# Kernel tuning notes

Hardware: AMD Instinct MI355X
Metric: run time of the kernel (lower is better)

## Reference

```python
import jax, jax.numpy as jnp
import numpy as np
from jax import lax

B, C, H, W = 4, 256, 64, 64
R = 4  # reduction
BN_EPS = 1e-5


def setup_inputs() -> dict:
    key = jax.random.key(0)
    ks = jax.random.split(key, 18)
    n = jax.random.normal
    return {
        "x_self": n(ks[0], (B, C, H, W), jnp.float32),
        "x_other": n(ks[1], (B, C, H, W), jnp.float32),
        "q_w": n(ks[2], (C, C), jnp.float32) * 0.05,      # self_q 1x1 conv
        "q_b": n(ks[3], (C,), jnp.float32) * 0.05,
        "kv_w": n(ks[4], (2 * C, C), jnp.float32) * 0.05,  # other_kv 1x1 conv
        "kv_b": n(ks[5], (2 * C,), jnp.float32) * 0.05,
        "g1_w": n(ks[6], (C // R, C), jnp.float32) * 0.05,  # gate conv1
        "g1_b": n(ks[7], (C // R,), jnp.float32) * 0.05,
        "g2_w": n(ks[8], (1, C // R), jnp.float32) * 0.05,  # gate conv2
        "g2_b": n(ks[9], (1,), jnp.float32) * 0.05,
        "dw_w": n(ks[10], (C, 1, 3, 3), jnp.float32) * 0.1,  # depthwise 3x3
        "dw_b": n(ks[11], (C,), jnp.float32) * 0.05,
        "bn_g": jnp.ones((C,), jnp.float32),
        "bn_b": jnp.zeros((C,), jnp.float32),
        "bn_m": n(ks[12], (C,), jnp.float32) * 0.05,
        "bn_v": jax.random.uniform(ks[13], (C,), jnp.float32, 0.5, 1.5),
        "out_w": n(ks[14], (C, C), jnp.float32) * 0.05,
        "out_b": n(ks[15], (C,), jnp.float32) * 0.05,
    }


def _conv1x1(x, w, b):
    return jnp.einsum('bchw,oc->bohw', x, w) + b[None, :, None, None]


def reference(x_self, x_other, q_w, q_b, kv_w, kv_b, g1_w, g1_b, g2_w, g2_b,
              dw_w, dw_b, bn_g, bn_b, bn_m, bn_v, out_w, out_b):
    # local branch: depthwise 3x3 conv -> BatchNorm (eval stats) -> SiLU
    y = lax.conv_general_dilated(
        x_self, dw_w, (1, 1), 'SAME',
        feature_group_count=C,
        dimension_numbers=('NCHW', 'OIHW', 'NCHW')) + dw_b[None, :, None, None]
    scale = (bn_g / jnp.sqrt(bn_v + BN_EPS))[None, :, None, None]
    y = (y - bn_m[None, :, None, None]) * scale + bn_b[None, :, None, None]
    local_feat = y * jax.nn.sigmoid(y)  # SiLU

    # cross attention over HW tokens
    q = _conv1x1(x_self, q_w, q_b).reshape(B, C, H * W)
    kv = _conv1x1(x_other, kv_w, kv_b)
    k = kv[:, :C].reshape(B, C, H * W)
    v = kv[:, C:].reshape(B, C, H * W)
    attn = jnp.einsum('bcn,bcm->bnm', q, k) / jnp.sqrt(jnp.float32(C))  # [B,HW,HW]
    attn = jax.nn.softmax(attn, axis=-1)
    attn_out = jnp.einsum('bnm,bcm->bcn', attn, v).reshape(B, C, H, W)

    # channel-squeeze gate on x_self -> scalar per sample
    p = jnp.mean(x_self, axis=(2, 3))                 # [B,C] global avg pool
    g = jax.nn.relu(p @ g1_w.T + g1_b)                # [B,C//R]
    g = jax.nn.sigmoid(g @ g2_w.T + g2_b)             # [B,1]
    gate = g[:, :, None, None]

    fused = local_feat + gate * attn_out
    return _conv1x1(fused, out_w, out_b)
```

## Files before the change

kernel.cpp:

```cpp
#include <hip/hip_runtime.h>
#include <stdint.h>

#define BB 4
#define CC 256
#define HH 64
#define WWD 64
#define NN 4096
#define LOG2E 1.4426950408889634f

typedef __attribute__((ext_vector_type(8))) short short8;
typedef __attribute__((ext_vector_type(4))) float f32x4;
typedef __attribute__((ext_vector_type(16))) float f32x16;
typedef __attribute__((ext_vector_type(4))) unsigned short us4;
typedef unsigned long long ull;

__device__ __forceinline__ unsigned short f2bf(float f) {
  unsigned int u = __float_as_uint(f);
  u += 0x7fffu + ((u >> 16) & 1u);
  return (unsigned short)(u >> 16);
}
__device__ __forceinline__ float bf2f(unsigned short h) {
  return __uint_as_float(((unsigned int)h) << 16);
}
__device__ __forceinline__ short8 ld8(const unsigned short* p) {
  return *reinterpret_cast<const short8*>(p);
}
__device__ __forceinline__ unsigned char f2fp8(float v) {
  return (unsigned char)__builtin_amdgcn_cvt_pk_fp8_f32(v, v, 0, false);
}
__device__ __forceinline__ int rowmap(int reg, int h) {
  return (reg & 3) + 8 * (reg >> 2) + 4 * h;
}

__global__ __launch_bounds__(256, 2) void k_pre(
    const float* __restrict__ xs, const float* __restrict__ xo,
    const float* __restrict__ dww, const float* __restrict__ dwb,
    const float* __restrict__ bng, const float* __restrict__ bnb,
    const float* __restrict__ bnm, const float* __restrict__ bnv,
    const float* __restrict__ qw, const float* __restrict__ kvw,
    const float* __restrict__ ow, unsigned short* __restrict__ XtS,
    unsigned short* __restrict__ XtO, unsigned short* __restrict__ localT,
    float* __restrict__ psumA, unsigned short* __restrict__ Wb) {
  __shared__ float rb3[3][64][67];
  __shared__ unsigned short sb[64][67];
  int tid = threadIdx.x;
  if (blockIdx.z == 8) {
    int i = (blockIdx.x * 64 + blockIdx.y) * 1024 + tid * 4;
    const float* src;
    if (i < 65536) src = qw + i;
    else if (i < 196608) src = kvw + (i - 65536);
    else src = ow + (i - 196608);
    f32x4 v = *reinterpret_cast<const f32x4*>(src);
    us4 r;
#pragma unroll
    for (int j = 0; j < 4; ++j) r[j] = f2bf(v[j]);
    *reinterpret_cast<us4*>(Wb + i) = r;
    return;
  }
  int c0 = blockIdx.x * 64, h = blockIdx.y;
  int b = blockIdx.z >> 1, which = blockIdx.z & 1;
  const float* src = which ? xo : xs;
  int wq = tid >> 6, w = tid & 63;
  int dlo = which ? 1 : 0, dhi = which ? 1 : 2;
  for (int d = dlo; d <= dhi; ++d) {
    int hh = h + d - 1;
    bool ok = (hh >= 0 && hh < HH);
#pragma unroll
    for (int p = 0; p < 4; ++p) {
      int idx = p * 256 + tid;
      int cl = idx >> 4, ws4 = (idx & 15) * 4;
      f32x4 v = {};
      if (ok)
        v = *reinterpret_cast<const f32x4*>(
            &src[(((size_t)(b * CC + c0 + cl)) * HH + hh) * WWD + ws4]);
#pragma unroll
      for (int j = 0; j < 4; ++j) rb3[d][cl][ws4 + 1 + j] = v[j];
    }
    if (tid < 64) { rb3[d][tid][0] = 0.f; rb3[d][tid][65] = 0.f; }
  }
  __syncthreads();
  unsigned short* dst = which ? XtO : XtS;
  int n0 = h * 64, cb = (tid & 15) * 4;
#pragma unroll
  for (int i = 0; i < 4; ++i) {
    int wl = i * 16 + (tid >> 4);
    us4 r;
#pragma unroll
    for (int j = 0; j < 4; ++j) r[j] = f2bf(rb3[1][cb + j][wl + 1]);
    *reinterpret_cast<us4*>(&dst[((size_t)b * NN + n0 + wl) * CC + c0 + cb]) = r;
  }
  if (which) return;
  if (tid < 64) {
    float s = 0.f;
    for (int ww = 0; ww < 64; ++ww) s += rb3[1][tid][ww + 1];
    psumA[((size_t)(b * 64 + h)) * CC + c0 + tid] = s;
  }
  for (int p = 0; p < 16; ++p) {
    int cl = p * 4 + wq, c = c0 + cl;
    float acc = 0.f;
#pragma unroll
    for (int di = 0; di < 3; ++di)
#pragma unroll
      for (int dj = 0; dj < 3; ++dj)
        acc = fmaf(rb3[di][cl][w + dj], dww[c * 9 + di * 3 + dj], acc);
    float y = acc + dwb[c];
    float sc = bng[c] * rsqrtf(bnv[c] + 1e-5f);
    float v = (y - bnm[c]) * sc + bnb[c];
    sb[cl][w] = f2bf(v / (1.f + __expf(-v)));
  }
  __syncthreads();
#pragma unroll
  for (int i = 0; i < 4; ++i) {
    int wl = i * 16 + (tid >> 4);
    us4 r;
#pragma unroll
    for (int j = 0; j < 4; ++j) r[j] = sb[cb + j][wl];
    *reinterpret_cast<us4*>(&localT[((size_t)b * NN + h * WWD + wl) * CC + c0 + cb]) = r;
  }
}

__global__ __launch_bounds__(256, 4) void k_qkv(
    const unsigned short* __restrict__ XtS, const unsigned short* __restrict__ XtO,
    const unsigned short* __restrict__ Wb, const float* __restrict__ qb,
    const float* __restrict__ kvb, const float* __restrict__ psumA,
    const float* __restrict__ g1w, const float* __restrict__ g1b,
    const float* __restrict__ g2w, const float* __restrict__ g2b,
    unsigned char* __restrict__ Qt8, unsigned char* __restrict__ Kt8,
    unsigned char* __restrict__ Vv8, float* __restrict__ gate) {
  __shared__ unsigned short Xs[64][264];
  int tid = threadIdx.x;
  int id = blockIdx.y;
  if (id == 3) {
    if (blockIdx.x != 0 || blockIdx.z != 0) return;
    float* mf = (float*)&Xs[0][0];
    float* hpf = mf + 1024;
    int c = tid;
    for (int b4 = 0; b4 < 4; ++b4) {
      float s = 0.f;
      for (int hh = 0; hh < 64; ++hh) s += psumA[((size_t)(b4 * 64 + hh)) * CC + c];
      mf[b4 * 256 + c] = s * (1.f / 4096.f);
    }
    __syncthreads();
    for (int b4 = 0; b4 < 4; ++b4) {
      int j = tid >> 2, cq = tid & 3;
      float s = 0.f;
      for (int cc = cq * 64; cc < cq * 64 + 64; ++cc)
        s = fmaf(mf[b4 * 256 + cc], g1w[j * CC + cc], s);
      hpf[j * 5 + cq] = s;
      __syncthreads();
      if (tid < 64) {
        float hh = fmaxf(hpf[tid * 5] + hpf[tid * 5 + 1] + hpf[tid * 5 + 2] +
                             hpf[tid * 5 + 3] + g1b[tid], 0.f);
        float t = hh * g2w[tid];
        for (int off = 32; off; off >>= 1) t += __shfl_down(t, off, 64);
        if (tid == 0) gate[b4] = 1.f / (1.f + expf(-(t + g2b[0])));
      }
      __syncthreads();
    }
    return;
  }
  int n0 = blockIdx.x * 64, b = blockIdx.z;
  const unsigned short* Xt = (id == 0) ? XtS : XtO;
  const unsigned short* W = Wb + id * 65536;
  int wave = tid >> 6, lane = tid & 63, l31 = lane & 31, h = lane >> 5;
#pragma unroll
  for (int p = 0; p < 8; ++p) {
    int r = p * 8 + (tid >> 5), c = (tid & 31) * 8;
    *reinterpret_cast<uint4*>(&Xs[r][c]) =
        *reinterpret_cast<const uint4*>(Xt + ((size_t)b * NN + n0 + r) * CC + c);
  }
  __syncthreads();
  int o0 = wave * 64;
  f32x16 acc[4] = {};
  if (id < 2) {
#pragma unroll
    for (int t = 0; t < 16; ++t) {
      short8 a0 = ld8(&Xs[l31][t * 16 + h * 8]);
      short8 a1 = ld8(&Xs[32 + l31][t * 16 + h * 8]);
      short8 b0 = ld8(W + (size_t)(o0 + l31) * CC + t * 16 + h * 8);
      short8 b1 = ld8(W + (size_t)(o0 + 32 + l31) * CC + t * 16 + h * 8);
      acc[0] = __builtin_amdgcn_mfma_f32_32x32x16_bf16(a0, b0, acc[0], 0, 0, 0);
      acc[1] = __builtin_amdgcn_mfma_f32_32x32x16_bf16(a0, b1, acc[1], 0, 0, 0);
      acc[2] = __builtin_amdgcn_mfma_f32_32x32x16_bf16(a1, b0, acc[2], 0, 0, 0);
      acc[3] = __builtin_amdgcn_mfma_f32_32x32x16_bf16(a1, b1, acc[3], 0, 0, 0);
    }
    const float* bias = id ? kvb : qb;
    unsigned char* Out8 = id ? Kt8 : Qt8;
    __syncthreads();
    unsigned char (*T8)[264] = reinterpret_cast<unsigned char(*)[264]>(&Xs[0][0]);
#pragma unroll
    for (int nt = 0; nt < 2; ++nt)
#pragma unroll
      for (int ot = 0; ot < 2; ++ot) {
        int o = o0 + ot * 32 + l31;
        float bv = bias[o];
#pragma unroll
        for (int reg = 0; reg < 16; ++reg) {
          int nl = nt * 32 + rowmap(reg, h);
          T8[nl][o] = f2fp8((acc[nt * 2 + ot][reg] + bv) * 0.25f);
        }
      }
    __syncthreads();
#pragma unroll
    for (int p = 0; p < 4; ++p) {
      int idx = p * 256 + tid, row = idx >> 4, cc = (idx & 15) * 16;
      ull a0 = *reinterpret_cast<const ull*>(&T8[row][cc]);
      ull a1 = *reinterpret_cast<const ull*>(&T8[row][cc + 8]);
      uint4 u;
      u.x = (unsigned)a0; u.y = (unsigned)(a0 >> 32);
      u.z = (unsigned)a1; u.w = (unsigned)(a1 >> 32);
      *reinterpret_cast<uint4*>(Out8 + ((size_t)b * NN + n0 + row) * CC + cc) = u;
    }
  } else {
#pragma unroll
    for (int t = 0; t < 16; ++t) {
      short8 a0 = ld8(W + (size_t)(o0 + l31) * CC + t * 16 + h * 8);
      short8 a1 = ld8(W + (size_t)(o0 + 32 + l31) * CC + t * 16 + h * 8);
      short8 b0 = ld8(&Xs[l31][t * 16 + h * 8]);
      short8 b1 = ld8(&Xs[32 + l31][t * 16 + h * 8]);
      acc[0] = __builtin_amdgcn_mfma_f32_32x32x16_bf16(a0, b0, acc[0], 0, 0, 0);
      acc[1] = __builtin_amdgcn_mfma_f32_32x32x16_bf16(a0, b1, acc[1], 0, 0, 0);
      acc[2] = __builtin_amdgcn_mfma_f32_32x32x16_bf16(a1, b0, acc[2], 0, 0, 0);
      acc[3] = __builtin_amdgcn_mfma_f32_32x32x16_bf16(a1, b1, acc[3], 0, 0, 0);
    }
    __syncthreads();
    unsigned char (*V8)[72] = reinterpret_cast<unsigned char(*)[72]>(&Xs[0][0]);
#pragma unroll
    for (int ot = 0; ot < 2; ++ot)
#pragma unroll
      for (int nt = 0; nt < 2; ++nt)
#pragma unroll
        for (int reg = 0; reg < 16; ++reg) {
          int o = o0 + ot * 32 + rowmap(reg, h);
          int nl = nt * 32 + l31;
          V8[o][nl] = f2fp8(acc[ot * 2 + nt][reg] + kvb[CC + o]);
        }
    __syncthreads();
#pragma unroll
    for (int p = 0; p < 4; ++p) {
      int idx = p * 256 + tid, o = idx >> 2, mm = (idx & 3) * 16;
      ull a0 = *reinterpret_cast<const ull*>(&V8[o][mm]);
      ull a1 = *reinterpret_cast<const ull*>(&V8[o][mm + 8]);
      uint4 u;
      u.x = (unsigned)a0; u.y = (unsigned)(a0 >> 32);
      u.z = (unsigned)a1; u.w = (unsigned)(a1 >> 32);
      *reinterpret_cast<uint4*>(Vv8 + ((size_t)b * CC + o) * NN + n0 + mm) = u;
    }
  }
}

__global__ __launch_bounds__(256, 3) void k_flash8(
    const unsigned char* __restrict__ Qt8, const unsigned char* __restrict__ Kt8,
    const unsigned char* __restrict__ Vv8, const unsigned short* __restrict__ localT,
    const float* __restrict__ gate, unsigned short* __restrict__ Opart16,
    float* __restrict__ Lpart, unsigned short* __restrict__ fusedT) {
  __shared__ unsigned char Ks8[64][264];
  __shared__ unsigned char Vs8[256][72];
  __shared__ unsigned char Ps8[64][72];
  __shared__ float lred[2][64];
  __shared__ float ltot[64];
  int b = blockIdx.x & 3, n0 = (blockIdx.x >> 2) * 64;
  int sp = blockIdx.y, nsp = gridDim.y;
  int tid = threadIdx.x, wave = tid >> 6, lane = tid & 63, l31 = lane & 31, h = lane >> 5;
  int rw = wave & 1, cw = wave >> 1;
  const unsigned char* qp = Qt8 + ((size_t)b * NN + n0 + rw * 32 + l31) * CC + h * 8;
  long qf[16];
#pragma unroll
  for (int t = 0; t < 16; ++t) qf[t] = *reinterpret_cast<const long*>(qp + t * 16);
  f32x16 O[4] = {};
  float lacc[16] = {};
  int m_lo = (64 * sp) / nsp, m_hi = (64 * (sp + 1)) / nsp;
  for (int mt = m_lo; mt < m_hi; ++mt) {
    int m0 = mt * 64;
    __syncthreads();
#pragma unroll
    for (int p = 0; p < 4; ++p) {
      int idx = p * 256 + tid, m = idx >> 4, cc = (idx & 15) * 16;
      const ull* gp = reinterpret_cast<const ull*>(Kt8 + ((size_t)b * NN + m0 + m) * CC + cc);
      ull a0 = gp[0], a1 = gp[1];
      *reinterpret_cast<ull*>(&Ks8[m][cc]) = a0;
      *reinterpret_cast<ull*>(&Ks8[m][cc + 8]) = a1;
    }
#pragma unroll
    for (int p = 0; p < 4; ++p) {
      int idx = p * 256 + tid, c = idx >> 2, mm = (idx & 3) * 16;
      const ull* gp = reinterpret_cast<const ull*>(Vv8 + ((size_t)b * CC + c) * NN + m0 + mm);
      ull a0 = gp[0], a1 = gp[1];
      *reinterpret_cast<ull*>(&Vs8[c][mm]) = a0;
      *reinterpret_cast<ull*>(&Vs8[c][mm + 8]) = a1;
    }
    __syncthreads();
    f32x16 S = {};
#pragma unroll
    for (int t = 0; t < 16; ++t) {
      long kf = *reinterpret_cast<const long*>(&Ks8[cw * 32 + l31][t * 16 + h * 8]);
      S = __builtin_amdgcn_mfma_f32_32x32x16_fp8_fp8(qf[t], kf, S, 0, 0, 0);
    }
#pragma unroll
    for (int reg = 0; reg < 16; ++reg) {
      float p = __builtin_exp2f(S[reg] * LOG2E);
      lacc[reg] += p;
      Ps8[rw * 32 + rowmap(reg, h)][cw * 32 + l31] = f2fp8(p);
    }
    __syncthreads();
#pragma unroll
    for (int t = 0; t < 4; ++t) {
      long pf = *reinterpret_cast<const long*>(&Ps8[rw * 32 + l31][t * 16 + h * 8]);
#pragma unroll
      for (int ct = 0; ct < 4; ++ct) {
        long vf = *reinterpret_cast<const long*>(&Vs8[cw * 128 + ct * 32 + l31][t * 16 + h * 8]);
        O[ct] = __builtin_amdgcn_mfma_f32_32x32x16_fp8_fp8(pf, vf, O[ct], 0, 0, 0);
      }
    }
  }
#pragma unroll
  for (int reg = 0; reg < 16; ++reg) {
    float v = lacc[reg];
#pragma unroll
    for (int msk = 1; msk < 32; msk <<= 1) v += __shfl_xor(v, msk, 64);
    lacc[reg] = v;
  }
  __syncthreads();
#pragma unroll
  for (int g = 0; g < 16; ++g)
    if (l31 == g) lred[cw][rw * 32 + rowmap(g, h)] = lacc[g];
  __syncthreads();
  size_t obase2 = (size_t)(b * nsp + sp) * NN;
  if (nsp == 1) {
    if (tid < 64) ltot[tid] = lred[0][tid] + lred[1][tid];
    __syncthreads();
    float gv = gate[b];
    float inv[16];
#pragma unroll
    for (int reg = 0; reg < 16; ++reg)
      inv[reg] = gv / ltot[rw * 32 + rowmap(reg, h)];
#pragma unroll
    for (int ct = 0; ct < 4; ++ct)
#pragma unroll
      for (int reg = 0; reg < 16; ++reg) {
        int n = n0 + rw * 32 + rowmap(reg, h);
        int c = cw * 128 + ct * 32 + l31;
        size_t idx = ((size_t)b * NN + n) * CC + c;
        fusedT[idx] = f2bf(bf2f(localT[idx]) + O[ct][reg] * inv[reg]);
      }
  } else {
    if (tid < 64) Lpart[obase2 + n0 + tid] = lred[0][tid] + lred[1][tid];
#pragma unroll
    for (int ct = 0; ct < 4; ++ct)
#pragma unroll
      for (int reg = 0; reg < 16; ++reg) {
        int n = n0 + rw * 32 + rowmap(reg, h);
        int c = cw * 128 + ct * 32 + l31;
        Opart16[(obase2 + n) * CC + c] = f2bf(O[ct][reg]);
      }
  }
}

__global__ __launch_bounds__(256, 4) void k_out(
    const unsigned short* __restrict__ W, const float* __restrict__ ob,
    const float* __restrict__ gate, const unsigned short* __restrict__ localT,
    const unsigned short* __restrict__ Opart16, const float* __restrict__ Lpart,
    const unsigned short* __restrict__ fusedT, float* __restrict__ out, int nsp) {
  __shared__ unsigned short Xs[64][264];
  int n0 = blockIdx.x * 64, o0 = blockIdx.y * 128, b = blockIdx.z;
  int tid = threadIdx.x, wave = tid >> 6, lane = tid & 63, l31 = lane & 31, h = lane >> 5;
  if (Opart16) {
    float gv = gate[b];
#pragma unroll
    for (int p = 0; p < 8; ++p) {
      int r = p * 8 + (tid >> 5), cc = (tid & 31) * 8;
      int n = n0 + r;
      float lsum = 0.f;
      for (int sp = 0; sp < nsp; ++sp) lsum += Lpart[(size_t)(b * nsp + sp) * NN + n];
      float g = gv / lsum;
      float ov[8] = {};
      for (int sp = 0; sp < nsp; ++sp) {
        short8 x = ld8(Opart16 + ((size_t)(b * nsp + sp) * NN + n) * CC + cc);
#pragma unroll
        for (int j = 0; j < 8; ++j) ov[j] += bf2f(((unsigned short*)&x)[j]);
      }
      const unsigned short* lp = localT + ((size_t)b * NN + n) * CC + cc;
      short8 lv = ld8(lp);
      us4 r0, r1;
#pragma unroll
      for (int j = 0; j < 4; ++j) {
        r0[j] = f2bf(bf2f(((unsigned short*)&lv)[j]) + ov[j] * g);
        r1[j] = f2bf(bf2f(((unsigned short*)&lv)[j + 4]) + ov[j + 4] * g);
      }
      *reinterpret_cast<us4*>(&Xs[r][cc]) = r0;
      *reinterpret_cast<us4*>(&Xs[r][cc + 4]) = r1;
    }
  } else {
#pragma unroll
    for (int p = 0; p < 8; ++p) {
      int r = p * 8 + (tid >> 5), c = (tid & 31) * 8;
      *reinterpret_cast<uint4*>(&Xs[r][c]) =
          *reinterpret_cast<const uint4*>(fusedT + ((size_t)b * NN + n0 + r) * CC + c);
    }
  }
  int obase = o0 + wave * 32;
  short8 af[16];
#pragma unroll
  for (int t = 0; t < 16; ++t) af[t] = ld8(W + (size_t)(obase + l31) * CC + t * 16 + h * 8);
  __syncthreads();
  f32x16 acc[2] = {};
#pragma unroll
  for (int t = 0; t < 16; ++t) {
    short8 b0 = ld8(&Xs[l31][t * 16 + h * 8]);
    short8 b1 = ld8(&Xs[32 + l31][t * 16 + h * 8]);
    acc[0] = __builtin_amdgcn_mfma_f32_32x32x16_bf16(af[t], b0, acc[0], 0, 0, 0);
    acc[1] = __builtin_amdgcn_mfma_f32_32x32x16_bf16(af[t], b1, acc[1], 0, 0, 0);
  }
#pragma unroll
  for (int nt = 0; nt < 2; ++nt)
#pragma unroll
    for (int reg = 0; reg < 16; ++reg) {
      int o = obase + rowmap(reg, h);
      int n = n0 + nt * 32 + l31;
      out[((size_t)b * CC + o) * NN + n] = acc[nt][reg] + ob[o];
    }
}

extern "C" void kernel_launch(void* const* d_in, const int* in_sizes, int n_in,
                              void* d_out, int out_size, void* d_ws, size_t ws_size,
                              hipStream_t stream) {
  const float* xs  = (const float*)d_in[0];
  const float* xo  = (const float*)d_in[1];
  const float* qw  = (const float*)d_in[2];
  const float* qb  = (const float*)d_in[3];
  const float* kvw = (const float*)d_in[4];
  const float* kvb = (const float*)d_in[5];
  const float* g1w = (const float*)d_in[6];
  const float* g1b = (const float*)d_in[7];
  const float* g2w = (const float*)d_in[8];
  const float* g2b = (const float*)d_in[9];
  const float* dww = (const float*)d_in[10];
  const float* dwb = (const float*)d_in[11];
  const float* bng = (const float*)d_in[12];
  const float* bnb = (const float*)d_in[13];
  const float* bnm = (const float*)d_in[14];
  const float* bnv = (const float*)d_in[15];
  const float* ow  = (const float*)d_in[16];
  const float* ob  = (const float*)d_in[17];
  float* out = (float*)d_out;
  char* ws = (char*)d_ws;

  const size_t SZ  = (size_t)BB * NN * CC * 2;
  const size_t SZ8 = (size_t)BB * NN * CC;
  unsigned short* XtS    = (unsigned short*)(ws);
  unsigned short* XtO    = (unsigned short*)(ws + SZ);
  unsigned short* localT = (unsigned short*)(ws + 2 * SZ);
  unsigned char*  Qt8    = (unsigned char*)(ws + 3 * SZ);
  unsigned char*  Kt8    = (unsigned char*)(ws + 3 * SZ + SZ8);
  unsigned char*  Vv8    = (unsigned char*)(ws + 3 * SZ + 2 * SZ8);
  unsigned short* Wb     = (unsigned short*)(ws + 3 * SZ + 3 * SZ8);
  float* psumA = (float*)(ws + 3 * SZ + 3 * SZ8 + 524288);
  float* gate  = (float*)(ws + 3 * SZ + 3 * SZ8 + 524288 + 262144);
  size_t tail  = 3 * SZ + 3 * SZ8 + 524288 + 262144 + 4096;
  float* Lpart = (float*)(ws + tail);
  unsigned short* Opart16 = (unsigned short*)(ws + tail + 262144);
  unsigned short* fusedT = XtS;

  size_t base = tail + 262144;
  int S = 1;
  if (ws_size >= base + 3ull * SZ) S = 3;
  else if (ws_size >= base + 2ull * SZ) S = 2;

  k_pre<<<dim3(4, 64, 9), 256, 0, stream>>>(xs, xo, dww, dwb, bng, bnb, bnm, bnv,
                                            qw, kvw, ow, XtS, XtO, localT, psumA, Wb);
  k_qkv<<<dim3(64, 4, 4), 256, 0, stream>>>(XtS, XtO, Wb, qb, kvb, psumA,
                                            g1w, g1b, g2w, g2b, Qt8, Kt8, Vv8, gate);
  k_flash8<<<dim3(256, S), 256, 0, stream>>>(Qt8, Kt8, Vv8, localT, gate, Opart16,
                                             Lpart, fusedT);
  k_out<<<dim3(64, 2, 4), 256, 0, stream>>>(Wb + 196608, ob, gate, localT,
                                            S > 1 ? Opart16 : nullptr, Lpart, fusedT,
                                            out, S);
}
```

Measured before the change: 253.4 us.

## Prefetch K/V tiles via async global-to-LDS loads with double-buffered V and swizzles

Flash attention now loads K and V tiles straight into LDS with global_load_lds. V is double-buffered and the next K tile is issued after the S computation, so memory traffic overlaps with MFMA work and there is one fewer barrier per iteration. The producer kernel writes K and V in an XOR-swizzled layout so the unpadded LDS tiles avoid bank conflicts. QK^T now uses swapped operands so each lane holds a whole row's partials. That turns the row-sum into a single cross-half shuffle and lets P be stored as packed fp8 words. It relies on exact wait-count and barrier ordering, so a mistake there could cause races.

```diff
diff --git a/kernel.cpp b/kernel.cpp
--- a/kernel.cpp
+++ b/kernel.cpp
@@ -30,6 +30,11 @@
 }
 __device__ __forceinline__ int rowmap(int reg, int h) {
   return (reg & 3) + 8 * (reg >> 2) + 4 * h;
+}
+__device__ __forceinline__ void gll16(const void* g, void* l) {
+  __builtin_amdgcn_global_load_lds(
+      (const __attribute__((address_space(1))) unsigned int*)g,
+      (__attribute__((address_space(3))) unsigned int*)l, 16, 0, 0);
 }
 
 __global__ __launch_bounds__(256, 2) void k_pre(
@@ -204,8 +209,9 @@
 #pragma unroll
     for (int p = 0; p < 4; ++p) {
       int idx = p * 256 + tid, row = idx >> 4, cc = (idx & 15) * 16;
-      ull a0 = *reinterpret_cast<const ull*>(&T8[row][cc]);
-      ull a1 = *reinterpret_cast<const ull*>(&T8[row][cc + 8]);
+      int s = (id == 1) ? ((row & 31) << 3) : 0;
+      ull a0 = *reinterpret_cast<const ull*>(&T8[row][cc ^ s]);
+      ull a1 = *reinterpret_cast<const ull*>(&T8[row][(cc + 8) ^ s]);
       uint4 u;
       u.x = (unsigned)a0; u.y = (unsigned)(a0 >> 32);
       u.z = (unsigned)a1; u.w = (unsigned)(a1 >> 32);
@@ -239,8 +245,9 @@
 #pragma unroll
     for (int p = 0; p < 4; ++p) {
       int idx = p * 256 + tid, o = idx >> 2, mm = (idx & 3) * 16;
-      ull a0 = *reinterpret_cast<const ull*>(&V8[o][mm]);
-      ull a1 = *reinterpret_cast<const ull*>(&V8[o][mm + 8]);
+      int s = (o & 7) << 3;
+      ull a0 = *reinterpret_cast<const ull*>(&V8[o][mm ^ s]);
+      ull a1 = *reinterpret_cast<const ull*>(&V8[o][(mm + 8) ^ s]);
       uint4 u;
       u.x = (unsigned)a0; u.y = (unsigned)(a0 >> 32);
       u.z = (unsigned)a1; u.w = (unsigned)(a1 >> 32);
@@ -254,79 +261,103 @@
     const unsigned char* __restrict__ Vv8, const unsigned short* __restrict__ localT,
     const float* __restrict__ gate, unsigned short* __restrict__ Opart16,
     float* __restrict__ Lpart, unsigned short* __restrict__ fusedT) {
-  __shared__ unsigned char Ks8[64][264];
-  __shared__ unsigned char Vs8[256][72];
+  __shared__ unsigned char Ks8[64][256];
+  __shared__ unsigned char Vs8[2][256][64];
   __shared__ unsigned char Ps8[64][72];
   __shared__ float lred[2][64];
-  __shared__ float ltot[64];
   int b = blockIdx.x & 3, n0 = (blockIdx.x >> 2) * 64;
   int sp = blockIdx.y, nsp = gridDim.y;
   int tid = threadIdx.x, wave = tid >> 6, lane = tid & 63, l31 = lane & 31, h = lane >> 5;
   int rw = wave & 1, cw = wave >> 1;
+  int wbase = tid & ~63;
   const unsigned char* qp = Qt8 + ((size_t)b * NN + n0 + rw * 32 + l31) * CC + h * 8;
   long qf[16];
 #pragma unroll
   for (int t = 0; t < 16; ++t) qf[t] = *reinterpret_cast<const long*>(qp + t * 16);
   f32x16 O[4] = {};
-  float lacc[16] = {};
+  float lsum = 0.f;
   int m_lo = (64 * sp) / nsp, m_hi = (64 * (sp + 1)) / nsp;
+  const unsigned char* Kbase = Kt8 + (size_t)b * NN * CC;
+  const unsigned char* Vbase = Vv8 + (size_t)b * CC * NN;
+  {
+    const unsigned char* Kg = Kbase + (size_t)(m_lo * 64) * CC;
+    const unsigned char* Vg = Vbase + m_lo * 64;
+    unsigned char* vdst = &Vs8[m_lo & 1][0][0];
+#pragma unroll
+    for (int p = 0; p < 4; ++p) {
+      int idx = p * 256 + tid;
+      int c = idx >> 2, mm = (idx & 3) * 16;
+      gll16(Vg + (size_t)c * NN + mm, vdst + (p * 256 + wbase) * 16);
+      gll16(Kg + (size_t)idx * 16, &Ks8[0][0] + (p * 256 + wbase) * 16);
+    }
+  }
+  const unsigned char* Krow = &Ks8[cw * 32 + l31][0];
+  int ksw = l31 << 3;
+  int vsw = (l31 & 7) << 3;
   for (int mt = m_lo; mt < m_hi; ++mt) {
-    int m0 = mt * 64;
-    __syncthreads();
-#pragma unroll
-    for (int p = 0; p < 4; ++p) {
-      int idx = p * 256 + tid, m = idx >> 4, cc = (idx & 15) * 16;
-      const ull* gp = reinterpret_cast<const ull*>(Kt8 + ((size_t)b * NN + m0 + m) * CC + cc);
-      ull a0 = gp[0], a1 = gp[1];
-      *reinterpret_cast<ull*>(&Ks8[m][cc]) = a0;
-      *reinterpret_cast<ull*>(&Ks8[m][cc + 8]) = a1;
-    }
-#pragma unroll
-    for (int p = 0; p < 4; ++p) {
-      int idx = p * 256 + tid, c = idx >> 2, mm = (idx & 3) * 16;
-      const ull* gp = reinterpret_cast<const ull*>(Vv8 + ((size_t)b * CC + c) * NN + m0 + mm);
-      ull a0 = gp[0], a1 = gp[1];
-      *reinterpret_cast<ull*>(&Vs8[c][mm]) = a0;
-      *reinterpret_cast<ull*>(&Vs8[c][mm + 8]) = a1;
-    }
-    __syncthreads();
+    asm volatile("s_waitcnt vmcnt(0)" ::: "memory");
+    __builtin_amdgcn_s_barrier();
+    __builtin_amdgcn_sched_barrier(0);
+    {
+      int mn = (mt + 1 < m_hi) ? mt + 1 : mt;
+      const unsigned char* Vg = Vbase + mn * 64;
+      unsigned char* vdst = &Vs8[(mt + 1) & 1][0][0];
+#pragma unroll
+      for (int p = 0; p < 4; ++p) {
+        int idx = p * 256 + tid;
+        int c = idx >> 2, mm = (idx & 3) * 16;
+        gll16(Vg + (size_t)c * NN + mm, vdst + (p * 256 + wbase) * 16);
+      }
+    }
+    __builtin_amdgcn_sched_barrier(0);
     f32x16 S = {};
 #pragma unroll
     for (int t = 0; t < 16; ++t) {
-      long kf = *reinterpret_cast<const long*>(&Ks8[cw * 32 + l31][t * 16 + h * 8]);
-      S = __builtin_amdgcn_mfma_f32_32x32x16_fp8_fp8(qf[t], kf, S, 0, 0, 0);
-    }
-#pragma unroll
-    for (int reg = 0; reg < 16; ++reg) {
-      float p = __builtin_exp2f(S[reg] * LOG2E);
-      lacc[reg] += p;
-      Ps8[rw * 32 + rowmap(reg, h)][cw * 32 + l31] = f2fp8(p);
-    }
-    __syncthreads();
+      long kf = *reinterpret_cast<const long*>(Krow + ((t * 16 + h * 8) ^ ksw));
+      S = __builtin_amdgcn_mfma_f32_32x32x16_fp8_fp8(kf, qf[t], S, 0, 0, 0);
+    }
+#pragma unroll
+    for (int r = 0; r < 4; ++r) {
+      float p0 = __builtin_exp2f(S[4 * r + 0] * LOG2E);
+      float p1 = __builtin_exp2f(S[4 * r + 1] * LOG2E);
+      float p2 = __builtin_exp2f(S[4 * r + 2] * LOG2E);
+      float p3 = __builtin_exp2f(S[4 * r + 3] * LOG2E);
+      lsum += (p0 + p1) + (p2 + p3);
+      unsigned u = __builtin_amdgcn_cvt_pk_fp8_f32(p0, p1, 0, false);
+      u = __builtin_amdgcn_cvt_pk_fp8_f32(p2, p3, u, true);
+      *reinterpret_cast<unsigned*>(&Ps8[rw * 32 + l31][cw * 32 + 8 * r + 4 * h]) = u;
+    }
+    asm volatile("s_waitcnt lgkmcnt(0)" ::: "memory");
+    __builtin_amdgcn_s_barrier();
+    __builtin_amdgcn_sched_barrier(0);
+    {
+      int mn = (mt + 1 < m_hi) ? mt + 1 : mt;
+      const unsigned char* Kg = Kbase + (size_t)(mn * 64) * CC;
+#pragma unroll
+      for (int p = 0; p < 4; ++p)
+        gll16(Kg + (size_t)(p * 256 + tid) * 16, &Ks8[0][0] + (p * 256 + wbase) * 16);
+    }
+    __builtin_amdgcn_sched_barrier(0);
+    const unsigned char (*Vc)[64] = Vs8[mt & 1];
 #pragma unroll
     for (int t = 0; t < 4; ++t) {
       long pf = *reinterpret_cast<const long*>(&Ps8[rw * 32 + l31][t * 16 + h * 8]);
 #pragma unroll
       for (int ct = 0; ct < 4; ++ct) {
-        long vf = *reinterpret_cast<const long*>(&Vs8[cw * 128 + ct * 32 + l31][t * 16 + h * 8]);
+        long vf = *reinterpret_cast<const long*>(
+            &Vc[cw * 128 + ct * 32 + l31][(t * 16 + h * 8) ^ vsw]);
         O[ct] = __builtin_amdgcn_mfma_f32_32x32x16_fp8_fp8(pf, vf, O[ct], 0, 0, 0);
       }
     }
   }
-#pragma unroll
-  for (int reg = 0; reg < 16; ++reg) {
-    float v = lacc[reg];
-#pragma unroll
-    for (int msk = 1; msk < 32; msk <<= 1) v += __shfl_xor(v, msk, 64);
-    lacc[reg] = v;
-  }
+  asm volatile("s_waitcnt vmcnt(0)" ::: "memory");
+  lsum += __shfl_xor(lsum, 32, 64);
   __syncthreads();
-#pragma unroll
-  for (int g = 0; g < 16; ++g)
-    if (l31 == g) lred[cw][rw * 32 + rowmap(g, h)] = lacc[g];
+  if (h == 0) lred[cw][rw * 32 + l31] = lsum;
   __syncthreads();
   size_t obase2 = (size_t)(b * nsp + sp) * NN;
   if (nsp == 1) {
+    float* ltot = reinterpret_cast<float*>(&Ps8[0][0]);
     if (tid < 64) ltot[tid] = lred[0][tid] + lred[1][tid];
     __syncthreads();
     float gv = gate[b];
```

Result: slower. 258.9 us (+2.2%).
